# Kernel optimization log

Measured on AMD Instinct MI355X. Metric: run time of the kernel, lower is better.

The kernel has to match this reference:

```python
import jax, jax.numpy as jnp
import numpy as np

B, D, S, H, A = 32768, 64, 16, 128, 17  # batch, obs_dim, num_skills, hidden, action_dim


def setup_inputs() -> dict:
    key = jax.random.key(0)
    ks = jax.random.split(key, 16)
    n = jax.random.normal
    inp = {
        "obs": n(ks[0], (B, D), dtype=jnp.float32),
        "skill_ids": jax.random.randint(ks[1], (B,), 0, S),
        # per-skill actor MLP params (stacked over skill axis)
        "Wa1": n(ks[2], (S, D, H), dtype=jnp.float32) * (1.0 / np.sqrt(D)),
        "ba1": jnp.zeros((S, H), dtype=jnp.float32),
        "Wa2": n(ks[3], (S, H, H), dtype=jnp.float32) * (1.0 / np.sqrt(H)),
        "ba2": jnp.zeros((S, H), dtype=jnp.float32),
        "Wa3": n(ks[4], (S, H, A), dtype=jnp.float32) * 0.01,
        "ba3": jnp.zeros((S, A), dtype=jnp.float32),
        # per-skill critic MLP params
        "Wc1": n(ks[5], (S, D, H), dtype=jnp.float32) * (1.0 / np.sqrt(D)),
        "bc1": jnp.zeros((S, H), dtype=jnp.float32),
        "Wc2": n(ks[6], (S, H, H), dtype=jnp.float32) * (1.0 / np.sqrt(H)),
        "bc2": jnp.zeros((S, H), dtype=jnp.float32),
        "Wc3": n(ks[7], (S, H, 1), dtype=jnp.float32) * (1.0 / np.sqrt(H)),
        "bc3": jnp.zeros((S, 1), dtype=jnp.float32),
    }
    return inp


def reference(obs, skill_ids, Wa1, ba1, Wa2, ba2, Wa3, ba3, Wc1, bc1, Wc2, bc2, Wc3, bc3):
    act = jnp.tanh
    num_skills = Wa1.shape[0]
    # dense evaluation of ALL skills' actor MLPs (faithful to original)
    ha = act(jnp.einsum('bd,sdh->bsh', obs, Wa1) + ba1)          # [B, S, H]
    ha = act(jnp.einsum('bsh,shk->bsk', ha, Wa2) + ba2)          # [B, S, H]
    logits_all = jnp.einsum('bsh,sha->bsa', ha, Wa3) + ba3       # [B, S, A]
    # dense evaluation of ALL skills' critic MLPs
    hc = act(jnp.einsum('bd,sdh->bsh', obs, Wc1) + bc1)
    hc = act(jnp.einsum('bsh,shk->bsk', hc, Wc2) + bc2)
    values_all = jnp.einsum('bsh,sho->bso', hc, Wc3) + bc3       # [B, S, 1]
    # one-hot gating select (discards S-1 of S computed outputs)
    gate = jax.nn.one_hot(skill_ids, num_skills, dtype=obs.dtype)  # [B, S]
    logits = jnp.sum(logits_all * gate[:, :, None], axis=1)       # [B, A]
    value = jnp.sum(values_all * gate[:, :, None], axis=1).squeeze(-1)  # [B]
    return logits, value
```

## Files before the change

### kernel.cpp

```cpp
#include <hip/hip_runtime.h>

#define Bt 32768
#define Dt 64
#define St 16
#define Ht 128
#define At 17

typedef __attribute__((ext_vector_type(8))) short bf16x8;
typedef __attribute__((ext_vector_type(4))) float f32x4;

#define CNT_OFF   0
#define PERM_OFF  128
#define WB_OFF    1049600
#define OA1 0
#define OA2 16384
#define OA3 49152
#define OC1 57344
#define OC2 73728
#define SKB 106496

__device__ __forceinline__ unsigned short f2bf(float f) {
  union { float f; unsigned u; } v; v.f = f;
  unsigned r = v.u + 0x7FFFu + ((v.u >> 16) & 1u);
  return (unsigned short)(r >> 16);
}

__device__ __forceinline__ unsigned cvtpk(float a, float b) {
  unsigned r;
  asm("v_cvt_pk_bf16_f32 %0, %1, %2" : "=v"(r) : "v"(a), "v"(b));
  return r;
}

__device__ __forceinline__ float tanh_fb(float acc, float b2) {
  const float t = __expf(__builtin_fmaf(acc, 2.0f, b2));
  const float r = __builtin_amdgcn_rcpf(t + 1.0f);
  return __builtin_fmaf(-2.0f, r, 1.0f);
}

__device__ __forceinline__ f32x4 MFMA(bf16x8 a, bf16x8 b, f32x4 c) {
  return __builtin_amdgcn_mfma_f32_16x16x32_bf16(a, b, c, 0, 0, 0);
}

#define LGKM0() asm volatile("s_waitcnt lgkmcnt(0)" ::: "memory")

__device__ __forceinline__ void ldsload16(const char* g, char* l) {
  __builtin_amdgcn_global_load_lds(
      (const __attribute__((address_space(1))) unsigned int*)g,
      (__attribute__((address_space(3))) unsigned int*)l, 16, 0, 0);
}
__device__ __forceinline__ void stageW(const char* g, char* lds, int bytes,
                                       int wave, int lane) {
  for (int c = wave * 1024; c < bytes; c += 4096)
    ldsload16(g + c + lane * 16, lds + c);
}

__global__ __launch_bounds__(256) void k_fused(
    const int* __restrict__ sid, unsigned short* __restrict__ perm,
    int* __restrict__ cnt,
    const float* __restrict__ Wa1, const float* __restrict__ Wa2,
    const float* __restrict__ Wa3, const float* __restrict__ Wc1,
    const float* __restrict__ Wc2, char* __restrict__ G) {
  __shared__ __align__(16) char smem[32768];
  const int tid = threadIdx.x;
  const int bid = blockIdx.x;

  if (bid >= 112) {
    int* lc = (int*)smem;
    int* lb = lc + St;
    const int b = (bid - 112) * 256 + tid;
    if (tid < St) lc[tid] = 0;
    __syncthreads();
    const int s = sid[b];
    const int p = atomicAdd(&lc[s], 1);
    __syncthreads();
    if (tid < St) lb[tid] = atomicAdd(&cnt[tid], lc[tid]);
    __syncthreads();
    perm[s * Bt + lb[s] + p] = (unsigned short)b;
    return;
  }

  const int s = bid / 7, t = bid % 7;
  char* Gs = G + s * SKB;

  if (t == 3) {
    const float* src = Wa3 + s * Ht * At;
    for (int e = tid; e < Ht * At; e += 256) {
      const int k = e / At, n = e - k * At;
      *(unsigned short*)(Gs + OA3 + n * 256 + ((2 * k) ^ ((n & 7) << 4))) =
          f2bf(src[e]);
    }
    return;
  }

  unsigned short* lds = (unsigned short*)smem;
  if (t == 0 || t == 4) {
    const float* src = (t == 0 ? Wa1 : Wc1) + s * Dt * Ht;
    const int off = (t == 0) ? OA1 : OC1;
    for (int it = 0; it < 8; ++it) {
      const int f = (it * 256 + tid) * 4;
      const int k = f >> 7, n0 = f & 127;
      const f32x4 v = *(const f32x4*)(src + f);
#pragma unroll
      for (int j = 0; j < 4; ++j) {
        const int n = n0 + j;
        const int byte = n * 128 + ((2 * k) ^ (((n >> 2) & 7) << 4));
        lds[byte >> 1] = f2bf(v[j]);
      }
    }
    __syncthreads();
    for (int it = 0; it < 8; ++it) {
      const int q = (it * 256 + tid) * 8;
      const int n = q >> 7, r = q & 127;
      const int srcoff = (r ^ ((n & 7) << 4)) ^ (((n >> 2) & 7) << 4);
      *(unsigned long long*)(Gs + off + q) =
          *(const unsigned long long*)(smem + n * 128 + srcoff);
    }
  } else {
    const bool isA = (t <= 2);
    const float* src = (isA ? Wa2 : Wc2) + s * Ht * Ht;
    const int off = isA ? OA2 : OC2;
    const int nhalf = ((t == 2) || (t == 6)) ? 64 : 0;
    for (int it = 0; it < 8; ++it) {
      const int e4 = it * 256 + tid;
      const int k = e4 >> 4, nl0 = (e4 & 15) * 4;
      const f32x4 v = *(const f32x4*)(src + k * 128 + nhalf + nl0);
#pragma unroll
      for (int j = 0; j < 4; ++j) {
        const int nl = nl0 + j;
        const int byte = nl * 256 + ((2 * k) ^ (((nl >> 2) & 15) << 4));
        lds[byte >> 1] = f2bf(v[j]);
      }
    }
    __syncthreads();
    for (int it = 0; it < 8; ++it) {
      const int q = (it * 256 + tid) * 8;
      const int nl = q >> 8, r = q & 255;
      const int srcoff = (r ^ ((nl & 7) << 4)) ^ (((nl >> 2) & 15) << 4);
      *(unsigned long long*)(Gs + off + (nhalf + nl) * 256 + r) =
          *(const unsigned long long*)(smem + nl * 256 + srcoff);
    }
  }
}

__device__ __forceinline__ bf16x8 wrd(const char* base, int srw, int n, int c,
                                      int lg, int msw) {
  return *(const bf16x8*)(base + n * srw + (((c) + lg * 16) ^ msw));
}

__device__ __forceinline__ void storeh(char* hw, int msw, int lg, int t,
                                       const f32x4 acc, const f32x4 b2) {
  const unsigned lo = cvtpk(tanh_fb(acc[0], b2[0]), tanh_fb(acc[1], b2[1]));
  const unsigned hi = cvtpk(tanh_fb(acc[2], b2[2]), tanh_fb(acc[3], b2[3]));
  *(unsigned long long*)(hw + ((32 * t + 8 * lg) ^ msw)) =
      (unsigned long long)lo | ((unsigned long long)hi << 32);
}

__device__ __forceinline__ void tile_actor(
    int tbase, int rnext, bool dopref, int& rowcur,
    f32x4& cx0, f32x4& cx1, f32x4& cx2, f32x4& cx3,
    const char* wbuf, char* hw, const float* obs,
    const f32x4 (&b1d)[8], const f32x4 (&b2d)[8], const f32x4 ba3v,
    const float ba316, float* out,
    int m, int lg, int msw, int wm, int cs) {
  union { bf16x8 v; unsigned u[4]; } XB0, XB1;
  XB0.u[0] = cvtpk(cx0[0], cx0[1]); XB0.u[1] = cvtpk(cx0[2], cx0[3]);
  XB0.u[2] = cvtpk(cx1[0], cx1[1]); XB0.u[3] = cvtpk(cx1[2], cx1[3]);
  XB1.u[0] = cvtpk(cx2[0], cx2[1]); XB1.u[1] = cvtpk(cx2[2], cx2[3]);
  XB1.u[2] = cvtpk(cx3[0], cx3[1]); XB1.u[3] = cvtpk(cx3[2], cx3[3]);
  const int myrow = rowcur;
  if (dopref) {
    const float* ap = obs + rnext * Dt + lg * 8;
    cx0 = *(const f32x4*)(ap);      cx1 = *(const f32x4*)(ap + 4);
    cx2 = *(const f32x4*)(ap + 32); cx3 = *(const f32x4*)(ap + 36);
  }
  rowcur = rnext;
#pragma unroll
  for (int nt = 0; nt < 8; ++nt) {
    const bf16x8 a0 = wrd(wbuf, 128, nt * 16 + m, 0, lg, msw);
    const bf16x8 a1 = wrd(wbuf, 128, nt * 16 + m, 64, lg, msw);
    f32x4 acc = {0.f, 0.f, 0.f, 0.f};
    acc = MFMA(a0, XB0.v, acc);
    acc = MFMA(a1, XB1.v, acc);
    storeh(hw, msw, lg, nt, acc, b1d[nt]);
  }
  LGKM0();
  const bf16x8 h0 = *(const bf16x8*)(hw + ((0   + 16 * lg) ^ msw));
  const bf16x8 h1 = *(const bf16x8*)(hw + ((64  + 16 * lg) ^ msw));
  const bf16x8 h2 = *(const bf16x8*)(hw + ((128 + 16 * lg) ^ msw));
  const bf16x8 h3 = *(const bf16x8*)(hw + ((192 + 16 * lg) ^ msw));
#pragma unroll
  for (int nt = 0; nt < 8; ++nt) {
    const int n = nt * 16 + m;
    const bf16x8 w0 = wrd(wbuf + 16384, 256, n, 0, lg, msw);
    const bf16x8 w1 = wrd(wbuf + 16384, 256, n, 64, lg, msw);
    const bf16x8 w2 = wrd(wbuf + 16384, 256, n, 128, lg, msw);
    const bf16x8 w3 = wrd(wbuf + 16384, 256, n, 192, lg, msw);
    f32x4 acc = {0.f, 0.f, 0.f, 0.f};
    acc = MFMA(w0, h0, acc); acc = MFMA(w1, h1, acc);
    acc = MFMA(w2, h2, acc); acc = MFMA(w3, h3, acc);
    storeh(hw, msw, lg, nt, acc, b2d[nt]);
  }
  LGKM0();
  const bf16x8 H0 = *(const bf16x8*)(hw + ((0   + 16 * lg) ^ msw));
  const bf16x8 H1 = *(const bf16x8*)(hw + ((64  + 16 * lg) ^ msw));
  const bf16x8 H2 = *(const bf16x8*)(hw + ((128 + 16 * lg) ^ msw));
  const bf16x8 H3 = *(const bf16x8*)(hw + ((192 + 16 * lg) ^ msw));
  const char* W3 = wbuf + 49152;
  const bf16x8 e0 = wrd(W3, 256, m, 0, lg, msw);
  const bf16x8 e1 = wrd(W3, 256, m, 64, lg, msw);
  const bf16x8 e2 = wrd(W3, 256, m, 128, lg, msw);
  const bf16x8 e3 = wrd(W3, 256, m, 192, lg, msw);
  const bf16x8 f0 = wrd(W3, 256, 16 + m, 0, lg, msw);
  const bf16x8 f1 = wrd(W3, 256, 16 + m, 64, lg, msw);
  const bf16x8 f2 = wrd(W3, 256, 16 + m, 128, lg, msw);
  const bf16x8 f3 = wrd(W3, 256, 16 + m, 192, lg, msw);
  f32x4 p0 = {0.f, 0.f, 0.f, 0.f}, p1 = {0.f, 0.f, 0.f, 0.f};
  p0 = MFMA(e0, H0, p0); p0 = MFMA(e1, H1, p0);
  p0 = MFMA(e2, H2, p0); p0 = MFMA(e3, H3, p0);
  p1 = MFMA(f0, H0, p1); p1 = MFMA(f1, H1, p1);
  p1 = MFMA(f2, H2, p1); p1 = MFMA(f3, H3, p1);
  if (tbase + wm < cs) {
    float* orow = out + myrow * At;
#pragma unroll
    for (int i = 0; i < 4; ++i)
      orow[4 * lg + i] = p0[i] + ba3v[i];
    if (lg == 0) orow[16] = p1[0] + ba316;
  }
}

__device__ __forceinline__ void tile_critic(
    int tbase, int rnext, bool dopref, int& rowcur,
    f32x4& cx0, f32x4& cx1, f32x4& cx2, f32x4& cx3,
    const char* wbuf, char* hw, const float* obs,
    const f32x4 (&b1d)[8], const f32x4 (&b2d)[8], const f32x4 (&wv)[8],
    const float bc3s, float* out,
    int m, int lg, int msw, int wm, int cs, int lane) {
  union { bf16x8 v; unsigned u[4]; } XB0, XB1;
  XB0.u[0] = cvtpk(cx0[0], cx0[1]); XB0.u[1] = cvtpk(cx0[2], cx0[3]);
  XB0.u[2] = cvtpk(cx1[0], cx1[1]); XB0.u[3] = cvtpk(cx1[2], cx1[3]);
  XB1.u[0] = cvtpk(cx2[0], cx2[1]); XB1.u[1] = cvtpk(cx2[2], cx2[3]);
  XB1.u[2] = cvtpk(cx3[0], cx3[1]); XB1.u[3] = cvtpk(cx3[2], cx3[3]);
  const int myrow = rowcur;
  if (dopref) {
    const float* ap = obs + rnext * Dt + lg * 8;
    cx0 = *(const f32x4*)(ap);      cx1 = *(const f32x4*)(ap + 4);
    cx2 = *(const f32x4*)(ap + 32); cx3 = *(const f32x4*)(ap + 36);
  }
  rowcur = rnext;
#pragma unroll
  for (int nt = 0; nt < 8; ++nt) {
    const bf16x8 a0 = wrd(wbuf, 128, nt * 16 + m, 0, lg, msw);
    const bf16x8 a1 = wrd(wbuf, 128, nt * 16 + m, 64, lg, msw);
    f32x4 acc = {0.f, 0.f, 0.f, 0.f};
    acc = MFMA(a0, XB0.v, acc);
    acc = MFMA(a1, XB1.v, acc);
    storeh(hw, msw, lg, nt, acc, b1d[nt]);
  }
  LGKM0();
  const bf16x8 h0 = *(const bf16x8*)(hw + ((0   + 16 * lg) ^ msw));
  const bf16x8 h1 = *(const bf16x8*)(hw + ((64  + 16 * lg) ^ msw));
  const bf16x8 h2 = *(const bf16x8*)(hw + ((128 + 16 * lg) ^ msw));
  const bf16x8 h3 = *(const bf16x8*)(hw + ((192 + 16 * lg) ^ msw));
  float vp = 0.f;
#pragma unroll
  for (int nt = 0; nt < 8; ++nt) {
    const int n = nt * 16 + m;
    const bf16x8 w0 = wrd(wbuf + 16384, 256, n, 0, lg, msw);
    const bf16x8 w1 = wrd(wbuf + 16384, 256, n, 64, lg, msw);
    const bf16x8 w2 = wrd(wbuf + 16384, 256, n, 128, lg, msw);
    const bf16x8 w3 = wrd(wbuf + 16384, 256, n, 192, lg, msw);
    f32x4 acc = {0.f, 0.f, 0.f, 0.f};
    acc = MFMA(w0, h0, acc); acc = MFMA(w1, h1, acc);
    acc = MFMA(w2, h2, acc); acc = MFMA(w3, h3, acc);
#pragma unroll
    for (int i = 0; i < 4; ++i)
      vp = __builtin_fmaf(tanh_fb(acc[i], b2d[nt][i]), wv[nt][i], vp);
  }
  vp += __shfl_xor(vp, 16);
  vp += __shfl_xor(vp, 32);
  if (lane < 16 && (tbase + wm < cs)) out[Bt * At + myrow] = vp + bc3s;
}

__global__ __launch_bounds__(256, 2) void k_main(
    const float* __restrict__ obs,
    const float* __restrict__ ba1, const float* __restrict__ ba2,
    const float* __restrict__ ba3, const float* __restrict__ bc1,
    const float* __restrict__ bc2, const float* __restrict__ Wc3,
    const float* __restrict__ bc3,
    const int* __restrict__ cnt, const unsigned short* __restrict__ perm,
    const char* __restrict__ G, float* __restrict__ out) {
  __shared__ __align__(16) char wbuf[57344];
  __shared__ __align__(16) char hbuf[16384];

  const int tid = threadIdx.x;
  const int wave = tid >> 6, lane = tid & 63;
  const int m = lane & 15, lg = lane >> 4;
  const bool actor = (blockIdx.x == 0);
  const int s = blockIdx.y, idx = blockIdx.z;
  const char* Gs = G + s * SKB;
  const int wm = wave * 16 + m;

  const unsigned short* pb = perm + s * Bt;
  int r0 = pb[idx * 64 + wm];
  int r1 = pb[(idx + 16) * 64 + wm];
  int r2 = pb[(idx + 32) * 64 + wm];
  const int cs = cnt[s];

  if (actor) {
    stageW(Gs + OA1, wbuf, 16384, wave, lane);
    stageW(Gs + OA2, wbuf + 16384, 32768, wave, lane);
    stageW(Gs + OA3, wbuf + 49152, 8192, wave, lane);
  } else {
    stageW(Gs + OC1, wbuf, 16384, wave, lane);
    stageW(Gs + OC2, wbuf + 16384, 32768, wave, lane);
  }

  r0 = min(r0, Bt - 1); r1 = min(r1, Bt - 1); r2 = min(r2, Bt - 1);
  const int ntl = (cs + 63) >> 6;

  f32x4 cx0, cx1, cx2, cx3;
  {
    const float* ap = obs + r0 * Dt + lg * 8;
    cx0 = *(const f32x4*)(ap);      cx1 = *(const f32x4*)(ap + 4);
    cx2 = *(const f32x4*)(ap + 32); cx3 = *(const f32x4*)(ap + 36);
  }

  char* hw = hbuf + wm * 256;
  const int msw = (m & 7) << 4;
  int rowcur = r0;

  if (actor) {
    f32x4 b1d[8], b2d[8];
#pragma unroll
    for (int nt = 0; nt < 8; ++nt) {
      const f32x4 t1 = *(const f32x4*)(ba1 + s * Ht + nt * 16 + lg * 4);
      const f32x4 t2 = *(const f32x4*)(ba2 + s * Ht + nt * 16 + lg * 4);
      b1d[nt] = t1 + t1;
      b2d[nt] = t2 + t2;
    }
    const f32x4 ba3v = *(const f32x4*)(ba3 + s * At + 4 * lg);
    const float ba316 = ba3[s * At + 16];
    __syncthreads();
    tile_actor(idx * 64, r1, true, rowcur, cx0, cx1, cx2, cx3,
               wbuf, hw, obs, b1d, b2d, ba3v, ba316, out, m, lg, msw, wm, cs);
    if (idx + 16 < ntl)
      tile_actor((idx + 16) * 64, r2, true, rowcur, cx0, cx1, cx2, cx3,
                 wbuf, hw, obs, b1d, b2d, ba3v, ba316, out, m, lg, msw, wm, cs);
    if (idx + 32 < ntl)
      tile_actor((idx + 32) * 64, r2, false, rowcur, cx0, cx1, cx2, cx3,
                 wbuf, hw, obs, b1d, b2d, ba3v, ba316, out, m, lg, msw, wm, cs);
  } else {
    f32x4 b1d[8], b2d[8], wv[8];
#pragma unroll
    for (int nt = 0; nt < 8; ++nt) {
      const f32x4 t1 = *(const f32x4*)(bc1 + s * Ht + nt * 16 + lg * 4);
      const f32x4 t2 = *(const f32x4*)(bc2 + s * Ht + nt * 16 + lg * 4);
      wv[nt] = *(const f32x4*)(Wc3 + s * Ht + nt * 16 + lg * 4);
      b1d[nt] = t1 + t1;
      b2d[nt] = t2 + t2;
    }
    const float bc3s = bc3[s];
    __syncthreads();
    tile_critic(idx * 64, r1, true, rowcur, cx0, cx1, cx2, cx3,
                wbuf, hw, obs, b1d, b2d, wv, bc3s, out, m, lg, msw, wm, cs, lane);
    if (idx + 16 < ntl)
      tile_critic((idx + 16) * 64, r2, true, rowcur, cx0, cx1, cx2, cx3,
                  wbuf, hw, obs, b1d, b2d, wv, bc3s, out, m, lg, msw, wm, cs, lane);
    if (idx + 32 < ntl)
      tile_critic((idx + 32) * 64, r2, false, rowcur, cx0, cx1, cx2, cx3,
                  wbuf, hw, obs, b1d, b2d, wv, bc3s, out, m, lg, msw, wm, cs, lane);
  }
}

extern "C" void kernel_launch(void* const* d_in, const int* in_sizes, int n_in,
                              void* d_out, int out_size, void* d_ws, size_t ws_size,
                              hipStream_t stream) {
  const float* obs = (const float*)d_in[0];
  const int* sid   = (const int*)d_in[1];
  const float* Wa1 = (const float*)d_in[2];
  const float* ba1 = (const float*)d_in[3];
  const float* Wa2 = (const float*)d_in[4];
  const float* ba2 = (const float*)d_in[5];
  const float* Wa3 = (const float*)d_in[6];
  const float* ba3 = (const float*)d_in[7];
  const float* Wc1 = (const float*)d_in[8];
  const float* bc1 = (const float*)d_in[9];
  const float* Wc2 = (const float*)d_in[10];
  const float* bc2 = (const float*)d_in[11];
  const float* Wc3 = (const float*)d_in[12];
  const float* bc3 = (const float*)d_in[13];
  float* out = (float*)d_out;
  char* ws = (char*)d_ws;

  int* cnt = (int*)(ws + CNT_OFF);
  unsigned short* perm = (unsigned short*)(ws + PERM_OFF);
  char* G = ws + WB_OFF;

  hipMemsetAsync(cnt, 0, St * sizeof(int), stream);
  k_fused<<<dim3(240), dim3(256), 0, stream>>>(sid, perm, cnt, Wa1, Wa2, Wa3, Wc1, Wc2, G);
  k_main<<<dim3(2, 16, 16), dim3(256), 0, stream>>>(
      obs, ba1, ba2, ba3, bc1, bc2, Wc3, bc3, cnt, perm, G, out);
}
```

Before: 26.09 us.

## Fuse bucketing and weight conversion into a single main kernel launch

Replaces the memset, the preprocessing kernel and the main kernel with one kernel. Each block scans its own 2048-row slice of skill ids to build a local row list in LDS, and converts its skill's fp32 weights to bf16 directly into LDS. This removes two launches and the global permutation/workspace round trip. In exchange every block redundantly converts weights (each skill's weights are converted 16 times). The blocks now loop over a variable number of tiles, so work per block depends on how the skill ids are distributed.

```diff
diff --git a/kernel.cpp b/kernel.cpp
--- a/kernel.cpp
+++ b/kernel.cpp
@@ -9,16 +9,6 @@
 typedef __attribute__((ext_vector_type(8))) short bf16x8;
 typedef __attribute__((ext_vector_type(4))) float f32x4;
 
-#define CNT_OFF   0
-#define PERM_OFF  128
-#define WB_OFF    1049600
-#define OA1 0
-#define OA2 16384
-#define OA3 49152
-#define OC1 57344
-#define OC2 73728
-#define SKB 106496
-
 __device__ __forceinline__ unsigned short f2bf(float f) {
   union { float f; unsigned u; } v; v.f = f;
   unsigned r = v.u + 0x7FFFu + ((v.u >> 16) & 1u);
@@ -42,105 +32,6 @@
 }
 
 #define LGKM0() asm volatile("s_waitcnt lgkmcnt(0)" ::: "memory")
-
-__device__ __forceinline__ void ldsload16(const char* g, char* l) {
-  __builtin_amdgcn_global_load_lds(
-      (const __attribute__((address_space(1))) unsigned int*)g,
-      (__attribute__((address_space(3))) unsigned int*)l, 16, 0, 0);
-}
-__device__ __forceinline__ void stageW(const char* g, char* lds, int bytes,
-                                       int wave, int lane) {
-  for (int c = wave * 1024; c < bytes; c += 4096)
-    ldsload16(g + c + lane * 16, lds + c);
-}
-
-__global__ __launch_bounds__(256) void k_fused(
-    const int* __restrict__ sid, unsigned short* __restrict__ perm,
-    int* __restrict__ cnt,
-    const float* __restrict__ Wa1, const float* __restrict__ Wa2,
-    const float* __restrict__ Wa3, const float* __restrict__ Wc1,
-    const float* __restrict__ Wc2, char* __restrict__ G) {
-  __shared__ __align__(16) char smem[32768];
-  const int tid = threadIdx.x;
-  const int bid = blockIdx.x;
-
-  if (bid >= 112) {
-    int* lc = (int*)smem;
-    int* lb = lc + St;
-    const int b = (bid - 112) * 256 + tid;
-    if (tid < St) lc[tid] = 0;
-    __syncthreads();
-    const int s = sid[b];
-    const int p = atomicAdd(&lc[s], 1);
-    __syncthreads();
-    if (tid < St) lb[tid] = atomicAdd(&cnt[tid], lc[tid]);
-    __syncthreads();
-    perm[s * Bt + lb[s] + p] = (unsigned short)b;
-    return;
-  }
-
-  const int s = bid / 7, t = bid % 7;
-  char* Gs = G + s * SKB;
-
-  if (t == 3) {
-    const float* src = Wa3 + s * Ht * At;
-    for (int e = tid; e < Ht * At; e += 256) {
-      const int k = e / At, n = e - k * At;
-      *(unsigned short*)(Gs + OA3 + n * 256 + ((2 * k) ^ ((n & 7) << 4))) =
-          f2bf(src[e]);
-    }
-    return;
-  }
-
-  unsigned short* lds = (unsigned short*)smem;
-  if (t == 0 || t == 4) {
-    const float* src = (t == 0 ? Wa1 : Wc1) + s * Dt * Ht;
-    const int off = (t == 0) ? OA1 : OC1;
-    for (int it = 0; it < 8; ++it) {
-      const int f = (it * 256 + tid) * 4;
-      const int k = f >> 7, n0 = f & 127;
-      const f32x4 v = *(const f32x4*)(src + f);
-#pragma unroll
-      for (int j = 0; j < 4; ++j) {
-        const int n = n0 + j;
-        const int byte = n * 128 + ((2 * k) ^ (((n >> 2) & 7) << 4));
-        lds[byte >> 1] = f2bf(v[j]);
-      }
-    }
-    __syncthreads();
-    for (int it = 0; it < 8; ++it) {
-      const int q = (it * 256 + tid) * 8;
-      const int n = q >> 7, r = q & 127;
-      const int srcoff = (r ^ ((n & 7) << 4)) ^ (((n >> 2) & 7) << 4);
-      *(unsigned long long*)(Gs + off + q) =
-          *(const unsigned long long*)(smem + n * 128 + srcoff);
-    }
-  } else {
-    const bool isA = (t <= 2);
-    const float* src = (isA ? Wa2 : Wc2) + s * Ht * Ht;
-    const int off = isA ? OA2 : OC2;
-    const int nhalf = ((t == 2) || (t == 6)) ? 64 : 0;
-    for (int it = 0; it < 8; ++it) {
-      const int e4 = it * 256 + tid;
-      const int k = e4 >> 4, nl0 = (e4 & 15) * 4;
-      const f32x4 v = *(const f32x4*)(src + k * 128 + nhalf + nl0);
-#pragma unroll
-      for (int j = 0; j < 4; ++j) {
-        const int nl = nl0 + j;
-        const int byte = nl * 256 + ((2 * k) ^ (((nl >> 2) & 15) << 4));
-        lds[byte >> 1] = f2bf(v[j]);
-      }
-    }
-    __syncthreads();
-    for (int it = 0; it < 8; ++it) {
-      const int q = (it * 256 + tid) * 8;
-      const int nl = q >> 8, r = q & 255;
-      const int srcoff = (r ^ ((nl & 7) << 4)) ^ (((nl >> 2) & 15) << 4);
-      *(unsigned long long*)(Gs + off + (nhalf + nl) * 256 + r) =
-          *(const unsigned long long*)(smem + nl * 256 + srcoff);
-    }
-  }
-}
 
 __device__ __forceinline__ bf16x8 wrd(const char* base, int srw, int n, int c,
                                       int lg, int msw) {
@@ -281,53 +172,87 @@
   if (lane < 16 && (tbase + wm < cs)) out[Bt * At + myrow] = vp + bc3s;
 }
 
-__global__ __launch_bounds__(256, 2) void k_main(
-    const float* __restrict__ obs,
-    const float* __restrict__ ba1, const float* __restrict__ ba2,
-    const float* __restrict__ ba3, const float* __restrict__ bc1,
-    const float* __restrict__ bc2, const float* __restrict__ Wc3,
-    const float* __restrict__ bc3,
-    const int* __restrict__ cnt, const unsigned short* __restrict__ perm,
-    const char* __restrict__ G, float* __restrict__ out) {
+__global__ __launch_bounds__(256, 2) void k_all(
+    const float* __restrict__ obs, const int* __restrict__ sid,
+    const float* __restrict__ Wa1, const float* __restrict__ ba1,
+    const float* __restrict__ Wa2, const float* __restrict__ ba2,
+    const float* __restrict__ Wa3, const float* __restrict__ ba3,
+    const float* __restrict__ Wc1, const float* __restrict__ bc1,
+    const float* __restrict__ Wc2, const float* __restrict__ bc2,
+    const float* __restrict__ Wc3, const float* __restrict__ bc3,
+    float* __restrict__ out) {
   __shared__ __align__(16) char wbuf[57344];
   __shared__ __align__(16) char hbuf[16384];
+  __shared__ unsigned short rlist[2048];
+  __shared__ int rcnt;
 
   const int tid = threadIdx.x;
   const int wave = tid >> 6, lane = tid & 63;
   const int m = lane & 15, lg = lane >> 4;
   const bool actor = (blockIdx.x == 0);
   const int s = blockIdx.y, idx = blockIdx.z;
-  const char* Gs = G + s * SKB;
   const int wm = wave * 16 + m;
 
-  const unsigned short* pb = perm + s * Bt;
-  int r0 = pb[idx * 64 + wm];
-  int r1 = pb[(idx + 16) * 64 + wm];
-  int r2 = pb[(idx + 32) * 64 + wm];
-  const int cs = cnt[s];
-
-  if (actor) {
-    stageW(Gs + OA1, wbuf, 16384, wave, lane);
-    stageW(Gs + OA2, wbuf + 16384, 32768, wave, lane);
-    stageW(Gs + OA3, wbuf + 49152, 8192, wave, lane);
-  } else {
-    stageW(Gs + OC1, wbuf, 16384, wave, lane);
-    stageW(Gs + OC2, wbuf + 16384, 32768, wave, lane);
-  }
-
-  r0 = min(r0, Bt - 1); r1 = min(r1, Bt - 1); r2 = min(r2, Bt - 1);
+  if (tid == 0) rcnt = 0;
+  __syncthreads();
+
+  const int ebase = idx * 2048;
+#pragma unroll
+  for (int r = 0; r < 8; ++r) {
+    const int e = ebase + r * 256 + tid;
+    const bool p = (sid[e] == s);
+    const unsigned long long mk = __ballot(p);
+    int wb = 0;
+    if (lane == 0) wb = atomicAdd(&rcnt, (int)__popcll(mk));
+    wb = __shfl(wb, 0);
+    if (p) rlist[wb + (int)__popcll(mk & ((1ULL << lane) - 1ULL))] =
+        (unsigned short)e;
+  }
+  __syncthreads();
+  const int cs = rcnt;
+  const int cm1 = (cs > 0) ? cs - 1 : 0;
   const int ntl = (cs + 63) >> 6;
 
-  f32x4 cx0, cx1, cx2, cx3;
-  {
-    const float* ap = obs + r0 * Dt + lg * 8;
+  f32x4 cx0 = {}, cx1 = {}, cx2 = {}, cx3 = {};
+  int rowcur = 0;
+  if (cs > 0) {
+    rowcur = rlist[min(wm, cm1)];
+    const float* ap = obs + rowcur * Dt + lg * 8;
     cx0 = *(const f32x4*)(ap);      cx1 = *(const f32x4*)(ap + 4);
     cx2 = *(const f32x4*)(ap + 32); cx3 = *(const f32x4*)(ap + 36);
   }
 
+  {
+    const float* W1s = (actor ? Wa1 : Wc1) + s * Dt * Ht;
+    const float* W2s = (actor ? Wa2 : Wc2) + s * Ht * Ht;
+#pragma unroll
+    for (int i = 0; i < 16; ++i) {
+      const int w = i * 256 + tid;
+      const int n = w & 127, kp = w >> 7;
+      const unsigned u =
+          cvtpk(W1s[(2 * kp) * Ht + n], W1s[(2 * kp + 1) * Ht + n]);
+      *(unsigned*)(wbuf + n * 128 + ((4 * kp) ^ ((n & 7) << 4))) = u;
+    }
+#pragma unroll
+    for (int i = 0; i < 32; ++i) {
+      const int w = i * 256 + tid;
+      const int n = w & 127, kp = w >> 7;
+      const unsigned u =
+          cvtpk(W2s[(2 * kp) * Ht + n], W2s[(2 * kp + 1) * Ht + n]);
+      *(unsigned*)(wbuf + 16384 + n * 256 + ((4 * kp) ^ ((n & 7) << 4))) = u;
+    }
+    if (actor) {
+      const float* W3s = Wa3 + s * Ht * At;
+      for (int e = tid; e < Ht * At; e += 256) {
+        const int k = e / At, n = e - k * At;
+        *(unsigned short*)(wbuf + 49152 + n * 256 +
+                           ((2 * k) ^ ((n & 7) << 4))) = f2bf(W3s[e]);
+      }
+    }
+  }
+
   char* hw = hbuf + wm * 256;
   const int msw = (m & 7) << 4;
-  int rowcur = r0;
 
   if (actor) {
     f32x4 b1d[8], b2d[8];
@@ -341,14 +266,11 @@
     const f32x4 ba3v = *(const f32x4*)(ba3 + s * At + 4 * lg);
     const float ba316 = ba3[s * At + 16];
     __syncthreads();
-    tile_actor(idx * 64, r1, true, rowcur, cx0, cx1, cx2, cx3,
-               wbuf, hw, obs, b1d, b2d, ba3v, ba316, out, m, lg, msw, wm, cs);
-    if (idx + 16 < ntl)
-      tile_actor((idx + 16) * 64, r2, true, rowcur, cx0, cx1, cx2, cx3,
+    for (int t = 0; t < ntl; ++t) {
+      const int rn = rlist[min((t + 1) * 64 + wm, cm1)];
+      tile_actor(t * 64, rn, t + 1 < ntl, rowcur, cx0, cx1, cx2, cx3,
                  wbuf, hw, obs, b1d, b2d, ba3v, ba316, out, m, lg, msw, wm, cs);
-    if (idx + 32 < ntl)
-      tile_actor((idx + 32) * 64, r2, false, rowcur, cx0, cx1, cx2, cx3,
-                 wbuf, hw, obs, b1d, b2d, ba3v, ba316, out, m, lg, msw, wm, cs);
+    }
   } else {
     f32x4 b1d[8], b2d[8], wv[8];
 #pragma unroll
@@ -361,14 +283,12 @@
     }
     const float bc3s = bc3[s];
     __syncthreads();
-    tile_critic(idx * 64, r1, true, rowcur, cx0, cx1, cx2, cx3,
-                wbuf, hw, obs, b1d, b2d, wv, bc3s, out, m, lg, msw, wm, cs, lane);
-    if (idx + 16 < ntl)
-      tile_critic((idx + 16) * 64, r2, true, rowcur, cx0, cx1, cx2, cx3,
-                  wbuf, hw, obs, b1d, b2d, wv, bc3s, out, m, lg, msw, wm, cs, lane);
-    if (idx + 32 < ntl)
-      tile_critic((idx + 32) * 64, r2, false, rowcur, cx0, cx1, cx2, cx3,
-                  wbuf, hw, obs, b1d, b2d, wv, bc3s, out, m, lg, msw, wm, cs, lane);
+    for (int t = 0; t < ntl; ++t) {
+      const int rn = rlist[min((t + 1) * 64 + wm, cm1)];
+      tile_critic(t * 64, rn, t + 1 < ntl, rowcur, cx0, cx1, cx2, cx3,
+                  wbuf, hw, obs, b1d, b2d, wv, bc3s, out, m, lg, msw, wm, cs,
+                  lane);
+    }
   }
 }
 
@@ -390,14 +310,8 @@
   const float* Wc3 = (const float*)d_in[12];
   const float* bc3 = (const float*)d_in[13];
   float* out = (float*)d_out;
-  char* ws = (char*)d_ws;
-
-  int* cnt = (int*)(ws + CNT_OFF);
-  unsigned short* perm = (unsigned short*)(ws + PERM_OFF);
-  char* G = ws + WB_OFF;
-
-  hipMemsetAsync(cnt, 0, St * sizeof(int), stream);
-  k_fused<<<dim3(240), dim3(256), 0, stream>>>(sid, perm, cnt, Wa1, Wa2, Wa3, Wc1, Wc2, G);
-  k_main<<<dim3(2, 16, 16), dim3(256), 0, stream>>>(
-      obs, ba1, ba2, ba3, bc1, bc2, Wc3, bc3, cnt, perm, G, out);
-}
+
+  k_all<<<dim3(2, 16, 16), dim3(256), 0, stream>>>(
+      obs, sid, Wa1, ba1, Wa2, ba2, Wa3, ba3, Wc1, bc1, Wc2, bc2, Wc3, bc3,
+      out);
+}
```

New measurement: 24.06 us (median of 2 runs). -7.8%, faster.
